# Performance work log

Hardware: AMD Instinct MI355X
Metric: run time of the kernel (lower is better)

The kernel has to match this reference:

```python
import jax, jax.numpy as jnp
import numpy as np

CELU_ALPHA = 3.0  # hardcoded in the torch module (nn.CELU(alpha=3.0), F.celu(alpha=3.0))

def celu(x):
    # celu(x, a) = max(0, x) + min(0, a*(exp(x/a)-1)); overflow-safe form
    return jnp.maximum(x, 0.0) + CELU_ALPHA * jnp.expm1(jnp.minimum(x, 0.0) / CELU_ALPHA)

def setup_inputs() -> dict:
    key = jax.random.key(0)
    k1, k2, k3, k4, k5 = jax.random.split(key, 5)
    N, E, H, D = 16384, 262144, 4, 64
    return {
        "features": jax.random.normal(k1, (N, D), dtype=jnp.float32),
        "metapath_embedding": jax.random.normal(k2, (E, D), dtype=jnp.float32),
        "attn1_w": jax.random.normal(k3, (H, D), dtype=jnp.float32) * 0.15,  # xavier-ish scale
        "attn2": jax.random.normal(k4, (H, D), dtype=jnp.float32) * 0.15,
        "segment_ids": jax.random.randint(k5, (E,), 0, N, dtype=jnp.int32),
    }

def reference(features, metapath_embedding, attn1_w, attn2, segment_ids):
    N, D = features.shape
    H = attn1_w.shape[0]
    # eft: same embedding broadcast over heads (torch.cat([emb]*H).view(-1,H,D))
    eft = celu(metapath_embedding)                    # [E, D]
    a1 = celu(features @ attn1_w.T)                   # [N, H] (per-node, shared across its instances)
    a2 = eft @ attn2.T                                # [E, H]
    a = celu(a1[segment_ids] + a2)                    # [E, H]
    # segment softmax over instances of each node
    m = jax.lax.stop_gradient(jax.ops.segment_max(a, segment_ids, num_segments=N))  # [N, H]
    ex = jnp.exp(a - m[segment_ids])                  # [E, H]
    denom = jax.ops.segment_sum(ex, segment_ids, num_segments=N)                    # [N, H]
    att = ex / denom[segment_ids]                     # [E, H]
    # weighted sum of eft over each node's instances -> [N, H, D]
    msg = jax.ops.segment_sum(att[:, :, None] * eft[:, None, :], segment_ids, num_segments=N)
    # empty segments yield 0 and celu(0)=0, matching the torch zero-fill branch
    return celu(msg).reshape(N, H * D)
```

## Files before the change

kernel.cpp:

```cpp
#include <hip/hip_runtime.h>
#include <math.h>

#define CAP 64
#define CSTRIDE 16

#define LOG2E    1.44269504088896341f
#define LOG2E_3  0.48089834696298780f

typedef float v2f __attribute__((ext_vector_type(2)));

__device__ __forceinline__ float celu3(float x) {
    return fmaxf(x, 0.0f) + 3.0f * (exp2f(fminf(x, 0.0f) * LOG2E_3) - 1.0f);
}

__device__ __forceinline__ v2f celu2(v2f x) {
    v2f zero = {0.f, 0.f};
    v2f pos = __builtin_elementwise_max(x, zero);
    v2f neg = __builtin_elementwise_min(x, zero);
    v2f targ = neg * LOG2E_3;
    v2f e;
    e.x = exp2f(targ.x);
    e.y = exp2f(targ.y);
    return (pos - 3.0f) + e * 3.0f;
}

template <int CTRL>
__device__ __forceinline__ float dpp_add(float v) {
    int o = __builtin_amdgcn_update_dpp(0, __float_as_int(v), CTRL, 0xf, 0xf, true);
    return v + __int_as_float(o);
}
template <int CTRL>
__device__ __forceinline__ float dpp_mov(float v) {
    int o = __builtin_amdgcn_update_dpp(0, __float_as_int(v), CTRL, 0xf, 0xf, true);
    return __int_as_float(o);
}
__device__ __forceinline__ float red16(float v) {
    v = dpp_add<0xB1>(v);
    v = dpp_add<0x4E>(v);
    v = dpp_add<0x124>(v);
    v = dpp_add<0x128>(v);
    return v;
}
__device__ __forceinline__ float wave_sum64(float v) {
    v = red16(v);
    v += __shfl_xor(v, 16, 64);
    v += __shfl_xor(v, 32, 64);
    return v;
}
__device__ __forceinline__ v2f xor_red2(v2f v) {
    v.x += __shfl_xor(v.x, 16); v.x += __shfl_xor(v.x, 32);
    v.y += __shfl_xor(v.y, 16); v.y += __shfl_xor(v.y, 32);
    return v;
}


__global__ __launch_bounds__(256) void init_kernel(
    int* __restrict__ counts, int N,
    const float* __restrict__ feat, const float* __restrict__ w1,
    float* __restrict__ a1)
{
    int nz = N * CSTRIDE;
    int nblk_zero = (nz + 255) / 256;
    if ((int)blockIdx.x < nblk_zero) {
        int i = blockIdx.x * 256 + threadIdx.x;
        if (i < nz) counts[i] = 0;
        return;
    }
    int n = (blockIdx.x - nblk_zero) * 4 + (threadIdx.x >> 6);
    int lane = threadIdx.x & 63;
    if (n >= N) return;
    float f = feat[(long)n * 64 + lane];
    float s[4];
#pragma unroll
    for (int h = 0; h < 4; ++h) s[h] = wave_sum64(f * w1[h * 64 + lane]);
    if (lane < 4) a1[n * 4 + lane] = celu3(s[lane]);
}


__global__ __launch_bounds__(256) void hist_kernel(
    const int* __restrict__ seg, int* __restrict__ counts,
    int* __restrict__ elist, int E)
{
    int i = blockIdx.x * 256 + threadIdx.x;
    int stride = gridDim.x * 256;
    for (; i < E; i += stride) {
        int s = seg[i];
        int r = atomicAdd(&counts[s * CSTRIDE], 1);
        if (r < CAP) elist[s * CAP + r] = i;
    }
}


__global__ __launch_bounds__(64) void fused_kernel(
    const float* __restrict__ meta, const float* __restrict__ w2,
    const float* __restrict__ a1, const int* __restrict__ counts,
    const int* __restrict__ elist, const int* __restrict__ seg,
    float* __restrict__ out, int N, int E)
{
    int lane = threadIdx.x;
    int n = blockIdx.x;
    if (n >= N) return;

    int cnt = counts[n * CSTRIDE];
    int g = lane >> 4;
    int q = lane & 15;
    int t = lane & 3;
    long ob = (long)n * 256 + g * 64 + q * 4;

    if (cnt == 0) {
        float4 z = {0.f, 0.f, 0.f, 0.f};
        *(float4*)(out + ob) = z;
        return;
    }

    float4 a1v = *(const float4*)(a1 + (long)n * 4);

    if (cnt <= CAP) {
        float4 w0 = *(const float4*)(w2 + 0 * 64 + q * 4);
        float4 w1v = *(const float4*)(w2 + 1 * 64 + q * 4);
        float4 wv2 = *(const float4*)(w2 + 2 * 64 + q * 4);
        float4 w3 = *(const float4*)(w2 + 3 * 64 + q * 4);
        v2f w0a = {w0.x, w0.y},  w0b = {w0.z, w0.w};
        v2f w1a = {w1v.x, w1v.y}, w1b = {w1v.z, w1v.w};
        v2f w2a = {wv2.x, wv2.y}, w2b = {wv2.z, wv2.w};
        v2f w3a = {w3.x, w3.y},  w3b = {w3.z, w3.w};

        float a1sel = (t == 0) ? a1v.x : (t == 1) ? a1v.y : (t == 2) ? a1v.z : a1v.w;

        int eid_l = (lane < cnt) ? elist[n * CAP + lane] : 0;
        const float* meta_q = meta + q * 4;

        float sp = 0.f;
        v2f acc0a = {0,0}, acc0b = {0,0}, acc1a = {0,0}, acc1b = {0,0};
        v2f acc2a = {0,0}, acc2b = {0,0}, acc3a = {0,0}, acc3b = {0,0};

        int nch = (cnt + 3) >> 2;
#pragma unroll 8
        for (int c = 0; c < nch; ++c) {
            int j = c * 4 + g;
            bool vr = j < cnt;
            int eid = __shfl(eid_l, j);
            float4 v = *(const float4*)(meta_q + (long)eid * 64);
            v2f va = {v.x, v.y}, vb = {v.z, v.w};
            v2f efa = celu2(va), efb = celu2(vb);

            v2f pd0 = efa * w0a + efb * w0b;
            v2f pd1 = efa * w1a + efb * w1b;
            v2f pd2 = efa * w2a + efb * w2b;
            v2f pd3 = efa * w3a + efb * w3b;
            float d0 = pd0.x + pd0.y;
            float d1 = pd1.x + pd1.y;
            float d2 = pd2.x + pd2.y;
            float d3 = pd3.x + pd3.y;

            d0 = dpp_add<0xB1>(d0); d1 = dpp_add<0xB1>(d1);
            d2 = dpp_add<0xB1>(d2); d3 = dpp_add<0xB1>(d3);
            d0 = dpp_add<0x4E>(d0); d1 = dpp_add<0x4E>(d1);
            d2 = dpp_add<0x4E>(d2); d3 = dpp_add<0x4E>(d3);
            float dsel = (t == 0) ? d0 : (t == 1) ? d1 : (t == 2) ? d2 : d3;
            dsel = dpp_add<0x124>(dsel);
            dsel = dpp_add<0x128>(dsel);

            float A = vr ? celu3(a1sel + dsel) : -INFINITY;
            float p = exp2f(fminf(A, 80.f) * LOG2E);
            sp += p;

            float b0 = dpp_mov<0x00>(p);
            float b1 = dpp_mov<0x55>(p);
            float b2 = dpp_mov<0xAA>(p);
            float b3 = dpp_mov<0xFF>(p);

            acc0a += efa * b0; acc0b += efb * b0;
            acc1a += efa * b1; acc1b += efb * b1;
            acc2a += efa * b2; acc2b += efb * b2;
            acc3a += efa * b3; acc3b += efb * b3;
        }

        sp += __shfl_xor(sp, 16); sp += __shfl_xor(sp, 32);

        acc0a = xor_red2(acc0a); acc0b = xor_red2(acc0b);
        acc1a = xor_red2(acc1a); acc1b = xor_red2(acc1b);
        acc2a = xor_red2(acc2a); acc2b = xor_red2(acc2b);
        acc3a = xor_red2(acc3a); acc3b = xor_red2(acc3b);

        float rg = 1.f / __int_as_float(__builtin_amdgcn_ds_bpermute(g << 2, __float_as_int(sp)));

        v2f ava = (g == 0) ? acc0a : (g == 1) ? acc1a : (g == 2) ? acc2a : acc3a;
        v2f avb = (g == 0) ? acc0b : (g == 1) ? acc1b : (g == 2) ? acc2b : acc3b;
        float4 o;
        o.x = celu3(ava.x * rg); o.y = celu3(ava.y * rg);
        o.z = celu3(avb.x * rg); o.w = celu3(avb.y * rg);
        *(float4*)(out + ob) = o;
        return;
    }

    {
        float a10 = a1v.x, a11 = a1v.y, a12 = a1v.z, a13 = a1v.w;
        float w2v0 = w2[0 * 64 + lane], w2v1 = w2[1 * 64 + lane];
        float w2v2 = w2[2 * 64 + lane], w2v3 = w2[3 * 64 + lane];
        float m0 = -INFINITY, m1 = -INFINITY, m2 = -INFINITY, m3 = -INFINITY;
        float s0 = 0.f, s1 = 0.f, s2 = 0.f, s3 = 0.f;
        float ac0 = 0.f, ac1 = 0.f, ac2 = 0.f, ac3 = 0.f;
        for (int base = 0; base < E; base += 64) {
            int e = base + lane;
            bool hit = (e < E) && (seg[e] == n);
            unsigned long long ball = __ballot(hit);
            while (ball) {
                int b = __ffsll((long long)ball) - 1;
                ball &= ball - 1;
                int eid = base + b;
                float eft = celu3(meta[(long)eid * 64 + lane]);
                float d0 = wave_sum64(eft * w2v0);
                float d1 = wave_sum64(eft * w2v1);
                float d2 = wave_sum64(eft * w2v2);
                float d3 = wave_sum64(eft * w2v3);
                float A0 = celu3(a10 + d0), A1 = celu3(a11 + d1);
                float A2 = celu3(a12 + d2), A3 = celu3(a13 + d3);
                float nm0 = fmaxf(m0, A0), nm1 = fmaxf(m1, A1);
                float nm2 = fmaxf(m2, A2), nm3 = fmaxf(m3, A3);
                float al0 = __expf(m0 - nm0), al1 = __expf(m1 - nm1);
                float al2 = __expf(m2 - nm2), al3 = __expf(m3 - nm3);
                float p0 = __expf(A0 - nm0), p1 = __expf(A1 - nm1);
                float p2 = __expf(A2 - nm2), p3 = __expf(A3 - nm3);
                s0 = fmaf(al0, s0, p0); s1 = fmaf(al1, s1, p1);
                s2 = fmaf(al2, s2, p2); s3 = fmaf(al3, s3, p3);
                ac0 = fmaf(p0, eft, al0 * ac0); ac1 = fmaf(p1, eft, al1 * ac1);
                ac2 = fmaf(p2, eft, al2 * ac2); ac3 = fmaf(p3, eft, al3 * ac3);
                m0 = nm0; m1 = nm1; m2 = nm2; m3 = nm3;
            }
        }
        long ob2 = (long)n * 256 + lane;
        out[ob2]       = celu3(ac0 / s0);
        out[ob2 + 64]  = celu3(ac1 / s1);
        out[ob2 + 128] = celu3(ac2 / s2);
        out[ob2 + 192] = celu3(ac3 / s3);
    }
}


extern "C" void kernel_launch(void* const* d_in, const int* in_sizes, int n_in,
                              void* d_out, int out_size, void* d_ws, size_t ws_size,
                              hipStream_t stream)
{
    const float* feat = (const float*)d_in[0];
    const float* meta = (const float*)d_in[1];
    const float* w1   = (const float*)d_in[2];
    const float* w2   = (const float*)d_in[3];
    const int*   seg  = (const int*)d_in[4];
    float* out = (float*)d_out;

    int N = in_sizes[0] / 64;
    int E = in_sizes[4];

    float* a1   = (float*)d_ws;
    int* counts = (int*)(a1 + (size_t)N * 4);
    int* elist  = counts + (size_t)N * CSTRIDE;

    int nblk_zero = (N * CSTRIDE + 255) / 256;
    int nblk_a1   = (N + 3) / 4;

    init_kernel<<<nblk_zero + nblk_a1, 256, 0, stream>>>(counts, N, feat, w1, a1);
    hist_kernel<<<512, 256, 0, stream>>>(seg, counts, elist, E);
    fused_kernel<<<N, 64, 0, stream>>>(meta, w2, a1, counts, elist, seg, out, N, E);
}
```

Baseline: 44.85 us.

## Process eight edges per wave step with eight lanes per 64-float row

Lane mapping in the fused per-node kernel changes so each edge row is handled by 8 lanes reading 8 floats each (two float4 loads), and 8 edges are processed per loop iteration instead of 4. This halves the iteration count and the per-edge dot-product reduction depth, which aims to raise memory-level parallelism on the gathered embedding rows. In exchange it doubles the accumulator registers, adds an extra cross-group shuffle stage to the final reductions, and only half the lanes write output.

```diff
diff --git a/kernel.cpp b/kernel.cpp
--- a/kernel.cpp
+++ b/kernel.cpp
@@ -12,7 +12,6 @@
 __device__ __forceinline__ float celu3(float x) {
     return fmaxf(x, 0.0f) + 3.0f * (exp2f(fminf(x, 0.0f) * LOG2E_3) - 1.0f);
 }
-
 __device__ __forceinline__ v2f celu2(v2f x) {
     v2f zero = {0.f, 0.f};
     v2f pos = __builtin_elementwise_max(x, zero);
@@ -47,9 +46,10 @@
     v += __shfl_xor(v, 32, 64);
     return v;
 }
-__device__ __forceinline__ v2f xor_red2(v2f v) {
-    v.x += __shfl_xor(v.x, 16); v.x += __shfl_xor(v.x, 32);
-    v.y += __shfl_xor(v.y, 16); v.y += __shfl_xor(v.y, 32);
+__device__ __forceinline__ v2f xor_red_g(v2f v) {
+    v.x += __shfl_xor(v.x, 8);  v.y += __shfl_xor(v.y, 8);
+    v.x += __shfl_xor(v.x, 16); v.y += __shfl_xor(v.y, 16);
+    v.x += __shfl_xor(v.x, 32); v.y += __shfl_xor(v.y, 32);
     return v;
 }
 
@@ -102,52 +102,61 @@
     if (n >= N) return;
 
     int cnt = counts[n * CSTRIDE];
-    int g = lane >> 4;
-    int q = lane & 15;
-    int t = lane & 3;
-    long ob = (long)n * 256 + g * 64 + q * 4;
+    int g8 = lane >> 3;
+    int o  = lane & 7;
+    int t  = lane & 3;
 
     if (cnt == 0) {
-        float4 z = {0.f, 0.f, 0.f, 0.f};
-        *(float4*)(out + ob) = z;
+        if (g8 < 4) {
+            long ob = (long)n * 256 + g8 * 64 + o * 8;
+            float4 z = {0.f, 0.f, 0.f, 0.f};
+            *(float4*)(out + ob) = z;
+            *(float4*)(out + ob + 4) = z;
+        }
         return;
     }
 
     float4 a1v = *(const float4*)(a1 + (long)n * 4);
 
     if (cnt <= CAP) {
-        float4 w0 = *(const float4*)(w2 + 0 * 64 + q * 4);
-        float4 w1v = *(const float4*)(w2 + 1 * 64 + q * 4);
-        float4 wv2 = *(const float4*)(w2 + 2 * 64 + q * 4);
-        float4 w3 = *(const float4*)(w2 + 3 * 64 + q * 4);
-        v2f w0a = {w0.x, w0.y},  w0b = {w0.z, w0.w};
-        v2f w1a = {w1v.x, w1v.y}, w1b = {w1v.z, w1v.w};
-        v2f w2a = {wv2.x, wv2.y}, w2b = {wv2.z, wv2.w};
-        v2f w3a = {w3.x, w3.y},  w3b = {w3.z, w3.w};
+        const float* w2o = w2 + o * 8;
+        float4 wA0 = *(const float4*)(w2o + 0 * 64), wB0 = *(const float4*)(w2o + 0 * 64 + 4);
+        float4 wA1 = *(const float4*)(w2o + 1 * 64), wB1 = *(const float4*)(w2o + 1 * 64 + 4);
+        float4 wA2 = *(const float4*)(w2o + 2 * 64), wB2 = *(const float4*)(w2o + 2 * 64 + 4);
+        float4 wA3 = *(const float4*)(w2o + 3 * 64), wB3 = *(const float4*)(w2o + 3 * 64 + 4);
+        v2f w0a = {wA0.x, wA0.y}, w0b = {wA0.z, wA0.w}, w0c = {wB0.x, wB0.y}, w0d = {wB0.z, wB0.w};
+        v2f w1a = {wA1.x, wA1.y}, w1b = {wA1.z, wA1.w}, w1c = {wB1.x, wB1.y}, w1d = {wB1.z, wB1.w};
+        v2f w2a = {wA2.x, wA2.y}, w2b = {wA2.z, wA2.w}, w2c = {wB2.x, wB2.y}, w2d = {wB2.z, wB2.w};
+        v2f w3a = {wA3.x, wA3.y}, w3b = {wA3.z, wA3.w}, w3c = {wB3.x, wB3.y}, w3d = {wB3.z, wB3.w};
 
         float a1sel = (t == 0) ? a1v.x : (t == 1) ? a1v.y : (t == 2) ? a1v.z : a1v.w;
 
         int eid_l = (lane < cnt) ? elist[n * CAP + lane] : 0;
-        const float* meta_q = meta + q * 4;
+        const float* meta_o = meta + o * 8;
 
         float sp = 0.f;
-        v2f acc0a = {0,0}, acc0b = {0,0}, acc1a = {0,0}, acc1b = {0,0};
-        v2f acc2a = {0,0}, acc2b = {0,0}, acc3a = {0,0}, acc3b = {0,0};
-
-        int nch = (cnt + 3) >> 2;
-#pragma unroll 8
+        v2f a0a = {0,0}, a0b = {0,0}, a0c = {0,0}, a0d = {0,0};
+        v2f a1a_ = {0,0}, a1b_ = {0,0}, a1c_ = {0,0}, a1d_ = {0,0};
+        v2f a2a = {0,0}, a2b = {0,0}, a2c = {0,0}, a2d = {0,0};
+        v2f a3a = {0,0}, a3b = {0,0}, a3c = {0,0}, a3d = {0,0};
+
+        int nch = (cnt + 7) >> 3;
+#pragma unroll 4
         for (int c = 0; c < nch; ++c) {
-            int j = c * 4 + g;
+            int j = c * 8 + g8;
             bool vr = j < cnt;
             int eid = __shfl(eid_l, j);
-            float4 v = *(const float4*)(meta_q + (long)eid * 64);
-            v2f va = {v.x, v.y}, vb = {v.z, v.w};
-            v2f efa = celu2(va), efb = celu2(vb);
-
-            v2f pd0 = efa * w0a + efb * w0b;
-            v2f pd1 = efa * w1a + efb * w1b;
-            v2f pd2 = efa * w2a + efb * w2b;
-            v2f pd3 = efa * w3a + efb * w3b;
+            const float* rp = meta_o + (long)eid * 64;
+            float4 va = *(const float4*)rp;
+            float4 vb = *(const float4*)(rp + 4);
+            v2f e0 = {va.x, va.y}, e1 = {va.z, va.w};
+            v2f e2 = {vb.x, vb.y}, e3 = {vb.z, vb.w};
+            e0 = celu2(e0); e1 = celu2(e1); e2 = celu2(e2); e3 = celu2(e3);
+
+            v2f pd0 = e0 * w0a + e1 * w0b + e2 * w0c + e3 * w0d;
+            v2f pd1 = e0 * w1a + e1 * w1b + e2 * w1c + e3 * w1d;
+            v2f pd2 = e0 * w2a + e1 * w2b + e2 * w2c + e3 * w2d;
+            v2f pd3 = e0 * w3a + e1 * w3b + e2 * w3c + e3 * w3d;
             float d0 = pd0.x + pd0.y;
             float d1 = pd1.x + pd1.y;
             float d2 = pd2.x + pd2.y;
@@ -158,8 +167,7 @@
             d0 = dpp_add<0x4E>(d0); d1 = dpp_add<0x4E>(d1);
             d2 = dpp_add<0x4E>(d2); d3 = dpp_add<0x4E>(d3);
             float dsel = (t == 0) ? d0 : (t == 1) ? d1 : (t == 2) ? d2 : d3;
-            dsel = dpp_add<0x124>(dsel);
-            dsel = dpp_add<0x128>(dsel);
+            dsel += __shfl_xor(dsel, 4, 64);
 
             float A = vr ? celu3(a1sel + dsel) : -INFINITY;
             float p = exp2f(fminf(A, 80.f) * LOG2E);
@@ -170,27 +178,40 @@
             float b2 = dpp_mov<0xAA>(p);
             float b3 = dpp_mov<0xFF>(p);
 
-            acc0a += efa * b0; acc0b += efb * b0;
-            acc1a += efa * b1; acc1b += efb * b1;
-            acc2a += efa * b2; acc2b += efb * b2;
-            acc3a += efa * b3; acc3b += efb * b3;
-        }
-
-        sp += __shfl_xor(sp, 16); sp += __shfl_xor(sp, 32);
-
-        acc0a = xor_red2(acc0a); acc0b = xor_red2(acc0b);
-        acc1a = xor_red2(acc1a); acc1b = xor_red2(acc1b);
-        acc2a = xor_red2(acc2a); acc2b = xor_red2(acc2b);
-        acc3a = xor_red2(acc3a); acc3b = xor_red2(acc3b);
-
-        float rg = 1.f / __int_as_float(__builtin_amdgcn_ds_bpermute(g << 2, __float_as_int(sp)));
-
-        v2f ava = (g == 0) ? acc0a : (g == 1) ? acc1a : (g == 2) ? acc2a : acc3a;
-        v2f avb = (g == 0) ? acc0b : (g == 1) ? acc1b : (g == 2) ? acc2b : acc3b;
-        float4 o;
-        o.x = celu3(ava.x * rg); o.y = celu3(ava.y * rg);
-        o.z = celu3(avb.x * rg); o.w = celu3(avb.y * rg);
-        *(float4*)(out + ob) = o;
+            a0a += e0 * b0; a0b += e1 * b0; a0c += e2 * b0; a0d += e3 * b0;
+            a1a_ += e0 * b1; a1b_ += e1 * b1; a1c_ += e2 * b1; a1d_ += e3 * b1;
+            a2a += e0 * b2; a2b += e1 * b2; a2c += e2 * b2; a2d += e3 * b2;
+            a3a += e0 * b3; a3b += e1 * b3; a3c += e2 * b3; a3d += e3 * b3;
+        }
+
+        sp += __shfl_xor(sp, 8); sp += __shfl_xor(sp, 16); sp += __shfl_xor(sp, 32);
+
+        a0a = xor_red_g(a0a); a0b = xor_red_g(a0b); a0c = xor_red_g(a0c); a0d = xor_red_g(a0d);
+        a1a_ = xor_red_g(a1a_); a1b_ = xor_red_g(a1b_); a1c_ = xor_red_g(a1c_); a1d_ = xor_red_g(a1d_);
+        a2a = xor_red_g(a2a); a2b = xor_red_g(a2b); a2c = xor_red_g(a2c); a2d = xor_red_g(a2d);
+        a3a = xor_red_g(a3a); a3b = xor_red_g(a3b); a3c = xor_red_g(a3c); a3d = xor_red_g(a3d);
+
+        float dd0 = dpp_mov<0x00>(sp);
+        float dd1 = dpp_mov<0x55>(sp);
+        float dd2 = dpp_mov<0xAA>(sp);
+        float dd3 = dpp_mov<0xFF>(sp);
+
+        if (g8 < 4) {
+            float dsel2 = (g8 == 0) ? dd0 : (g8 == 1) ? dd1 : (g8 == 2) ? dd2 : dd3;
+            float rg = 1.f / dsel2;
+            v2f r0 = (g8 == 0) ? a0a : (g8 == 1) ? a1a_ : (g8 == 2) ? a2a : a3a;
+            v2f r1 = (g8 == 0) ? a0b : (g8 == 1) ? a1b_ : (g8 == 2) ? a2b : a3b;
+            v2f r2 = (g8 == 0) ? a0c : (g8 == 1) ? a1c_ : (g8 == 2) ? a2c : a3c;
+            v2f r3 = (g8 == 0) ? a0d : (g8 == 1) ? a1d_ : (g8 == 2) ? a2d : a3d;
+            long ob = (long)n * 256 + g8 * 64 + o * 8;
+            float4 oA, oB;
+            oA.x = celu3(r0.x * rg); oA.y = celu3(r0.y * rg);
+            oA.z = celu3(r1.x * rg); oA.w = celu3(r1.y * rg);
+            oB.x = celu3(r2.x * rg); oB.y = celu3(r2.y * rg);
+            oB.z = celu3(r3.x * rg); oB.w = celu3(r3.y * rg);
+            *(float4*)(out + ob) = oA;
+            *(float4*)(out + ob + 4) = oB;
+        }
         return;
     }
 
```

Result: slower. 49.82 us (+11.1%).
